# Optimization experiments

Hardware: AMD Instinct MI355X
Metric: run time of the kernel (lower is better)

Reference implementation:

```python
import jax, jax.numpy as jnp
import numpy as np

NUM_HEADS = 16
NEG_FILL = -10000.0  # matches torch masked_fill value in source


def setup_inputs() -> dict:
    key = jax.random.key(0)
    ks = jax.random.split(key, 8)
    B, S, H = 4, 2048, 1024
    sc = 1.0 / np.sqrt(H)
    x = jax.random.normal(ks[0], (B, S, H), dtype=jnp.float32)
    L = jax.random.randint(ks[1], (B,), 1, S + 1, dtype=jnp.int64 if jax.config.jax_enable_x64 else jnp.int32)
    Wq = jax.random.normal(ks[2], (H, H), dtype=jnp.float32) * sc
    Wk = jax.random.normal(ks[3], (H, H), dtype=jnp.float32) * sc
    Wv = jax.random.normal(ks[4], (H, H), dtype=jnp.float32) * sc
    bv = jax.random.normal(ks[5], (H,), dtype=jnp.float32) * 0.01
    Wo = jax.random.normal(ks[6], (H, H), dtype=jnp.float32) * sc
    bo = jax.random.normal(ks[7], (H,), dtype=jnp.float32) * 0.01
    return {"x": x, "L": L, "Wq": Wq, "Wk": Wk, "Wv": Wv, "bv": bv, "Wo": Wo, "bo": bo}


def reference(x, L, Wq, Wk, Wv, bv, Wo, bo):
    # AttentionAggregator.forward with L given; dropout in eval mode (identity).
    B, S, H = x.shape
    nh = NUM_HEADS
    dk = H // nh
    # torch nn.Linear: y = x @ W.T + b
    q = (x @ Wq.T).reshape(B, S, nh, dk).transpose(0, 2, 1, 3)  # (B,h,S,dk)
    k = (x @ Wk.T).reshape(B, S, nh, dk).transpose(0, 2, 1, 3)
    v = (x @ Wv.T + bv).reshape(B, S, nh, dk).transpose(0, 2, 1, 3)
    scores = jnp.einsum("bhqd,bhkd->bhqk", q, k) / jnp.sqrt(jnp.float32(dk))
    valid = jnp.arange(S)[None, :] < L[:, None]  # (B,S) True where real token
    scores = jnp.where(valid[:, None, None, :], scores, NEG_FILL)
    attn = jax.nn.softmax(scores, axis=-1)
    ctx = jnp.einsum("bhqk,bhkd->bhqd", attn, v)
    ctx = ctx.transpose(0, 2, 1, 3).reshape(B, S, H)
    attn_out = ctx @ Wo.T + bo  # (B,S,H)
    # masked mean pool over valid positions
    m = valid.astype(x.dtype)  # (B,S)
    pooled = jnp.einsum("bsh,bs->bh", attn_out, m) / m.sum(axis=1, keepdims=True)
    return pooled
```

## Files before the change

kernel.cpp:

```cpp
#include <hip/hip_runtime.h>
#include <hip/hip_bf16.h>
#include <math.h>

constexpr int Bc = 4, Sc = 2048, Hc = 1024, NHc = 16, DKc = 64;

constexpr size_t XHOFF = 0;
constexpr size_t QOFF  = 4194304;
constexpr size_t KOFF  = 8388608;
constexpr size_t WQOFF = 12582912;
constexpr size_t WKOFF = 13107200;
constexpr size_t LIOFF = 13631488;
constexpr size_t WOFF  = 13762560;
constexpr size_t YOFF  = 13893632;
constexpr size_t CSOFF = 13959168;
constexpr size_t YPOFF = 13963264;
constexpr size_t RPOFF = 13963264;
constexpr size_t CPOFF = 13963264;

typedef __attribute__((ext_vector_type(8))) short bf16x8;
typedef __attribute__((ext_vector_type(4))) float f32x4;

__device__ inline short f2bf(float v) {
    __hip_bfloat16 h = __float2bfloat16(v);
    return *reinterpret_cast<short*>(&h);
}

__device__ inline float ex2(float x) {
#if defined(__has_builtin) && __has_builtin(__builtin_amdgcn_exp2f)
    return __builtin_amdgcn_exp2f(x);
#else
    float r; asm("v_exp_f32 %0, %1" : "=v"(r) : "v"(x)); return r;
#endif
}

__device__ inline void gld_lds16(const void* g, void* l) {
    __builtin_amdgcn_global_load_lds(
        (const __attribute__((address_space(1))) unsigned int*)g,
        (__attribute__((address_space(3))) unsigned int*)l, 16, 0, 0);
}

__global__ __launch_bounds__(256) void cvt_all_kernel(
    const float* __restrict__ x, const float* __restrict__ Wq,
    const float* __restrict__ Wk, float* __restrict__ ws)
{
    const size_t i = ((size_t)blockIdx.x * 256 + threadIdx.x) * 8;
    const float* src; short* dst; float scale; size_t off;
    constexpr float QSC = 0.125f * 1.44269504088896340736f;
    if (i < 8388608)       { src = x;  dst = (short*)(ws + XHOFF); off = i;            scale = 1.0f; }
    else if (i < 9437184)  { src = Wq; dst = (short*)(ws + WQOFF); off = i - 8388608;  scale = QSC;  }
    else                   { src = Wk; dst = (short*)(ws + WKOFF); off = i - 9437184;  scale = 1.0f; }
    float4 a = *(const float4*)(src + off);
    float4 b = *(const float4*)(src + off + 4);
    bf16x8 o;
    o[0] = f2bf(a.x * scale); o[1] = f2bf(a.y * scale);
    o[2] = f2bf(a.z * scale); o[3] = f2bf(a.w * scale);
    o[4] = f2bf(b.x * scale); o[5] = f2bf(b.y * scale);
    o[6] = f2bf(b.z * scale); o[7] = f2bf(b.w * scale);
    *(bf16x8*)(dst + off) = o;
}

__global__ __launch_bounds__(256) void proj_mfma_kernel(
    const int* __restrict__ L, float* __restrict__ ws)
{
    const int z  = blockIdx.z;
    const int m0 = blockIdx.y * 128;
    const int n0 = blockIdx.x * 128;
    const int b  = m0 >> 11;
    const int s0 = m0 & 2047;
    const int Lb = L[b];
    if (s0 >= Lb) return;

    const short* __restrict__ A = (const short*)(ws + XHOFF);
    const short* __restrict__ W = (const short*)(ws + (z == 0 ? WQOFF : WKOFF));
    short* __restrict__ Out = (short*)(ws + (z == 0 ? QOFF : KOFF));

    __shared__ __align__(16) short As[128 * 32];
    __shared__ __align__(16) short Bs[128 * 32];

    const int tid  = threadIdx.x;
    const int lane = tid & 63;
    const int wave = tid >> 6;
    const int l16  = lane & 15, quad = lane >> 4;
    const int wm = (wave & 1) * 64, wn = (wave >> 1) * 64;

    const int c0 = tid, c1 = tid + 256;
    const int r0 = c0 >> 2, g0 = (c0 & 3) * 8;
    const int r1 = c1 >> 2, g1 = (c1 & 3) * 8;
    short* lA0 = As + wave * 512;
    short* lA1 = As + 2048 + wave * 512;
    short* lB0 = Bs + wave * 512;
    short* lB1 = Bs + 2048 + wave * 512;

    const f32x4 z4 = {0.f, 0.f, 0.f, 0.f};
    f32x4 acc[4][4];
    #pragma unroll
    for (int i = 0; i < 4; ++i)
        #pragma unroll
        for (int j = 0; j < 4; ++j) acc[i][j] = z4;

    for (int k0 = 0; k0 < Hc; k0 += 32) {
        __syncthreads();
        gld_lds16(A + (size_t)(m0 + r0) * Hc + k0 + g0, lA0);
        gld_lds16(A + (size_t)(m0 + r1) * Hc + k0 + g1, lA1);
        gld_lds16(W + (size_t)(n0 + r0) * Hc + k0 + g0, lB0);
        gld_lds16(W + (size_t)(n0 + r1) * Hc + k0 + g1, lB1);
        __syncthreads();

        bf16x8 af[4], bfr[4];
        #pragma unroll
        for (int mt = 0; mt < 4; ++mt)
            af[mt] = *(const bf16x8*)(As + (wm + mt * 16 + l16) * 32 + quad * 8);
        #pragma unroll
        for (int nt = 0; nt < 4; ++nt)
            bfr[nt] = *(const bf16x8*)(Bs + (wn + nt * 16 + l16) * 32 + quad * 8);
        #pragma unroll
        for (int mt = 0; mt < 4; ++mt)
            #pragma unroll
            for (int nt = 0; nt < 4; ++nt)
                acc[mt][nt] = __builtin_amdgcn_mfma_f32_16x16x32_bf16(
                    af[mt], bfr[nt], acc[mt][nt], 0, 0, 0);
    }

    #pragma unroll
    for (int mt = 0; mt < 4; ++mt) {
        #pragma unroll
        for (int nt = 0; nt < 4; ++nt) {
            const int n = n0 + wn + nt * 16 + l16;
            const int h = n >> 6, d = n & 63;
            #pragma unroll
            for (int r = 0; r < 4; ++r) {
                const int s = s0 + wm + mt * 16 + quad * 4 + r;
                Out[(((size_t)b * NHc + h) * Sc + s) * DKc + d] =
                    f2bf(acc[mt][nt][r]);
            }
        }
    }
}

__global__ __launch_bounds__(256) void rowsum_part_kernel(
    const int* __restrict__ L, float* __restrict__ ws)
{
    const int bh = blockIdx.x;
    const int b  = bh >> 4;
    const int Lb = L[b];
    const int kc0 = blockIdx.z * 128;
    if (blockIdx.y * 128 >= Lb || kc0 >= Lb) return;

    const int tid  = threadIdx.x;
    const int wave = tid >> 6;
    const int lane = tid & 63;
    const int q0 = blockIdx.y * 128 + wave * 32;
    const int l16 = lane & 15, quad = lane >> 4;

    const short* __restrict__ qarr = (const short*)(ws + QOFF) + (size_t)bh * Sc * DKc;
    const short* __restrict__ karr = (const short*)(ws + KOFF) + (size_t)bh * Sc * DKc;

    __shared__ __align__(16) short Ks[128 * 64];

    const short* qrow0 = qarr + (size_t)(q0 + l16) * DKc;
    const short* qrow1 = qarr + (size_t)(q0 + 16 + l16) * DKc;
    const bf16x8 b0lo = *(const bf16x8*)(qrow0 + quad * 8);
    const bf16x8 b0hi = *(const bf16x8*)(qrow0 + 32 + quad * 8);
    const bf16x8 b1lo = *(const bf16x8*)(qrow1 + quad * 8);
    const bf16x8 b1hi = *(const bf16x8*)(qrow1 + 32 + quad * 8);

    #pragma unroll
    for (int i = 0; i < 4; ++i) {
        const int s = i * 256 + tid;
        const int row = s >> 3, cc = s & 7, c = cc ^ (row & 7);
        gld_lds16(karr + (size_t)(kc0 + row) * DKc + c * 8,
                  Ks + (i * 256 + wave * 64) * 8);
    }
    __syncthreads();

    float lacc0 = 0.f, lacc1 = 0.f;
    if (kc0 + 128 <= Lb) {
        #pragma unroll
        for (int t = 0; t < 8; ++t) {
            const int r = t * 16 + l16;
            const bf16x8 alo = *(const bf16x8*)(Ks + (r * 8 + (quad ^ (r & 7))) * 8);
            const bf16x8 ahi = *(const bf16x8*)(Ks + (r * 8 + ((4 + quad) ^ (r & 7))) * 8);
            f32x4 c0 = {0.f, 0.f, 0.f, 0.f}, c1 = {0.f, 0.f, 0.f, 0.f};
            c0 = __builtin_amdgcn_mfma_f32_16x16x32_bf16(alo, b0lo, c0, 0, 0, 0);
            c0 = __builtin_amdgcn_mfma_f32_16x16x32_bf16(ahi, b0hi, c0, 0, 0, 0);
            c1 = __builtin_amdgcn_mfma_f32_16x16x32_bf16(alo, b1lo, c1, 0, 0, 0);
            c1 = __builtin_amdgcn_mfma_f32_16x16x32_bf16(ahi, b1hi, c1, 0, 0, 0);
            const float e0 = ex2(c0[0]), e1 = ex2(c0[1]), e2 = ex2(c0[2]), e3 = ex2(c0[3]);
            const float f0 = ex2(c1[0]), f1 = ex2(c1[1]), f2 = ex2(c1[2]), f3 = ex2(c1[3]);
            lacc0 += (e0 + e1) + (e2 + e3);
            lacc1 += (f0 + f1) + (f2 + f3);
        }
    } else {
        #pragma unroll
        for (int t = 0; t < 8; ++t) {
            const int r = t * 16 + l16;
            const bf16x8 alo = *(const bf16x8*)(Ks + (r * 8 + (quad ^ (r & 7))) * 8);
            const bf16x8 ahi = *(const bf16x8*)(Ks + (r * 8 + ((4 + quad) ^ (r & 7))) * 8);
            f32x4 c0 = {0.f, 0.f, 0.f, 0.f}, c1 = {0.f, 0.f, 0.f, 0.f};
            c0 = __builtin_amdgcn_mfma_f32_16x16x32_bf16(alo, b0lo, c0, 0, 0, 0);
            c0 = __builtin_amdgcn_mfma_f32_16x16x32_bf16(ahi, b0hi, c0, 0, 0, 0);
            c1 = __builtin_amdgcn_mfma_f32_16x16x32_bf16(alo, b1lo, c1, 0, 0, 0);
            c1 = __builtin_amdgcn_mfma_f32_16x16x32_bf16(ahi, b1hi, c1, 0, 0, 0);
            #pragma unroll
            for (int rr = 0; rr < 4; ++rr) {
                const bool kv = (kc0 + t * 16 + quad * 4 + rr) < Lb;
                lacc0 += kv ? ex2(c0[rr]) : 0.f;
                lacc1 += kv ? ex2(c1[rr]) : 0.f;
            }
        }
    }
    lacc0 += __shfl_xor(lacc0, 16, 64); lacc0 += __shfl_xor(lacc0, 32, 64);
    lacc1 += __shfl_xor(lacc1, 16, 64); lacc1 += __shfl_xor(lacc1, 32, 64);
    float* __restrict__ rp = ws + RPOFF + ((size_t)blockIdx.z * 64 + bh) * Sc;
    if (quad == 0) rp[q0 + l16]      = lacc0;
    if (quad == 1) rp[q0 + 16 + l16] = lacc1;
}

__global__ __launch_bounds__(256) void rowsum_reduce_kernel(
    const int* __restrict__ L, float* __restrict__ ws)
{
    const int bh = blockIdx.y;
    const int q  = blockIdx.x * 256 + threadIdx.x;
    const int nc = (L[bh >> 4] + 127) >> 7;
    float acc = 0.f;
    for (int c = 0; c < nc; ++c)
        acc += ws[RPOFF + ((size_t)c * 64 + bh) * Sc + q];
    ws[LIOFF + (size_t)bh * Sc + q] = 1.0f / acc;
}

__global__ __launch_bounds__(256) void colsum_part_kernel(
    const int* __restrict__ L, float* __restrict__ ws)
{
    const int bh = blockIdx.x;
    const int b  = bh >> 4;
    const int Lb = L[b];
    const int qc0 = blockIdx.z * 128;
    if (blockIdx.y * 128 >= Lb || qc0 >= Lb) return;

    const int tid  = threadIdx.x;
    const int wave = tid >> 6;
    const int lane = tid & 63;
    const int k0 = blockIdx.y * 128 + wave * 32;
    const int l16 = lane & 15, quad = lane >> 4;

    const short* __restrict__ qarr = (const short*)(ws + QOFF) + (size_t)bh * Sc * DKc;
    const short* __restrict__ karr = (const short*)(ws + KOFF) + (size_t)bh * Sc * DKc;
    const float* __restrict__ liarr = ws + LIOFF + (size_t)bh * Sc;

    __shared__ __align__(16) short Qs[128 * 64];
    __shared__ __align__(16) float Lis[128];

    const short* krow0 = karr + (size_t)(k0 + l16) * DKc;
    const short* krow1 = karr + (size_t)(k0 + 16 + l16) * DKc;
    const bf16x8 a0lo = *(const bf16x8*)(krow0 + quad * 8);
    const bf16x8 a0hi = *(const bf16x8*)(krow0 + 32 + quad * 8);
    const bf16x8 a1lo = *(const bf16x8*)(krow1 + quad * 8);
    const bf16x8 a1hi = *(const bf16x8*)(krow1 + 32 + quad * 8);

    #pragma unroll
    for (int i = 0; i < 4; ++i) {
        const int s = i * 256 + tid;
        const int row = s >> 3, cc = s & 7, c = cc ^ (row & 7);
        gld_lds16(qarr + (size_t)(qc0 + row) * DKc + c * 8,
                  Qs + (i * 256 + wave * 64) * 8);
    }
    if (tid < 32)
        gld_lds16(liarr + qc0 + tid * 4, Lis);
    __syncthreads();

    float w0[4] = {0.f, 0.f, 0.f, 0.f};
    float w1[4] = {0.f, 0.f, 0.f, 0.f};

    if (qc0 + 128 <= Lb) {
        #pragma unroll
        for (int t = 0; t < 8; ++t) {
            const int r = t * 16 + l16;
            const bf16x8 blo = *(const bf16x8*)(Qs + (r * 8 + (quad ^ (r & 7))) * 8);
            const bf16x8 bhi = *(const bf16x8*)(Qs + (r * 8 + ((4 + quad) ^ (r & 7))) * 8);
            const float lv = Lis[r];
            f32x4 c0 = {0.f, 0.f, 0.f, 0.f}, c1 = {0.f, 0.f, 0.f, 0.f};
            c0 = __builtin_amdgcn_mfma_f32_16x16x32_bf16(a0lo, blo, c0, 0, 0, 0);
            c0 = __builtin_amdgcn_mfma_f32_16x16x32_bf16(a0hi, bhi, c0, 0, 0, 0);
            c1 = __builtin_amdgcn_mfma_f32_16x16x32_bf16(a1lo, blo, c1, 0, 0, 0);
            c1 = __builtin_amdgcn_mfma_f32_16x16x32_bf16(a1hi, bhi, c1, 0, 0, 0);
            #pragma unroll
            for (int rr = 0; rr < 4; ++rr) {
                w0[rr] += ex2(c0[rr]) * lv;
                w1[rr] += ex2(c1[rr]) * lv;
            }
        }
    } else {
        #pragma unroll
        for (int t = 0; t < 8; ++t) {
            const int r = t * 16 + l16;
            const bf16x8 blo = *(const bf16x8*)(Qs + (r * 8 + (quad ^ (r & 7))) * 8);
            const bf16x8 bhi = *(const bf16x8*)(Qs + (r * 8 + ((4 + quad) ^ (r & 7))) * 8);
            const float lv = (qc0 + r < Lb) ? Lis[r] : 0.f;
            f32x4 c0 = {0.f, 0.f, 0.f, 0.f}, c1 = {0.f, 0.f, 0.f, 0.f};
            c0 = __builtin_amdgcn_mfma_f32_16x16x32_bf16(a0lo, blo, c0, 0, 0, 0);
            c0 = __builtin_amdgcn_mfma_f32_16x16x32_bf16(a0hi, bhi, c0, 0, 0, 0);
            c1 = __builtin_amdgcn_mfma_f32_16x16x32_bf16(a1lo, blo, c1, 0, 0, 0);
            c1 = __builtin_amdgcn_mfma_f32_16x16x32_bf16(a1hi, bhi, c1, 0, 0, 0);
            #pragma unroll
            for (int rr = 0; rr < 4; ++rr) {
                w0[rr] += ex2(c0[rr]) * lv;
                w1[rr] += ex2(c1[rr]) * lv;
            }
        }
    }
    #pragma unroll
    for (int off = 1; off <= 8; off <<= 1) {
        #pragma unroll
        for (int rr = 0; rr < 4; ++rr) {
            w0[rr] += __shfl_xor(w0[rr], off, 64);
            w1[rr] += __shfl_xor(w1[rr], off, 64);
        }
    }
    if (l16 == 0) {
        float* __restrict__ cp = ws + CPOFF + ((size_t)blockIdx.z * 64 + bh) * Sc;
        #pragma unroll
        for (int rr = 0; rr < 4; ++rr) {
            cp[k0 + quad * 4 + rr]      = w0[rr];
            cp[k0 + 16 + quad * 4 + rr] = w1[rr];
        }
    }
}

__global__ __launch_bounds__(256) void colsum_reduce_kernel(
    const int* __restrict__ L, float* __restrict__ ws)
{
    const int bh = blockIdx.y;
    const int k  = blockIdx.x * 256 + threadIdx.x;
    const int nc = (L[bh >> 4] + 127) >> 7;
    float acc = 0.f;
    for (int c = 0; c < nc; ++c)
        acc += ws[CPOFF + ((size_t)c * 64 + bh) * Sc + k];
    ws[WOFF + (size_t)bh * Sc + k] = acc;
}

__global__ __launch_bounds__(256) void yw_part_kernel(
    const float* __restrict__ x, const int* __restrict__ L,
    float* __restrict__ ws)
{
    const int b  = blockIdx.y;
    const int j0 = blockIdx.x * 64;
    const int s0 = blockIdx.z * 128;
    const int Lb = L[b];
    if (s0 >= Lb) return;
    const int js = threadIdx.x & 63;
    const int sl = threadIdx.x >> 6;
    const float* __restrict__ warr = ws + WOFF + (size_t)b * NHc * Sc;
    const float* __restrict__ xb = x + (size_t)b * Sc * Hc;

    __shared__ float wt[128][20];
    __shared__ float red[4][16][64];

    #pragma unroll
    for (int i = 0; i < 8; ++i) {
        const int s = (threadIdx.x & 15) + 16 * i;
        const int h = threadIdx.x >> 4;
        float v = 0.f;
        if (s0 + s < Lb) v = warr[(size_t)h * Sc + s0 + s];
        wt[s][h] = v;
    }
    __syncthreads();

    float acc[16];
    #pragma unroll
    for (int h = 0; h < 16; ++h) acc[h] = 0.f;

    #pragma unroll 4
    for (int s = sl; s < 128; s += 4) {
        const float xv = xb[(size_t)(s0 + s) * Hc + j0 + js];
        const f32x4 wa = *(const f32x4*)&wt[s][0];
        const f32x4 wb = *(const f32x4*)&wt[s][4];
        const f32x4 wc = *(const f32x4*)&wt[s][8];
        const f32x4 wd = *(const f32x4*)&wt[s][12];
        #pragma unroll
        for (int h = 0; h < 4; ++h) acc[h]      += wa[h] * xv;
        #pragma unroll
        for (int h = 0; h < 4; ++h) acc[4 + h]  += wb[h] * xv;
        #pragma unroll
        for (int h = 0; h < 4; ++h) acc[8 + h]  += wc[h] * xv;
        #pragma unroll
        for (int h = 0; h < 4; ++h) acc[12 + h] += wd[h] * xv;
    }
    #pragma unroll
    for (int h = 0; h < 16; ++h) red[sl][h][js] = acc[h];
    __syncthreads();
    if (sl == 0) {
        float* __restrict__ yp = ws + YPOFF +
            ((size_t)blockIdx.z * Bc * NHc + (size_t)b * NHc) * Hc;
        #pragma unroll
        for (int h = 0; h < 16; ++h)
            yp[(size_t)h * Hc + j0 + js] =
                red[0][h][js] + red[1][h][js] + red[2][h][js] + red[3][h][js];
    }
}

__global__ __launch_bounds__(256) void yw_reduce_kernel(
    const int* __restrict__ L, float* __restrict__ ws)
{
    const int b = blockIdx.y;
    const int i = blockIdx.x * 256 + threadIdx.x;
    const int nc = (L[b] + 127) >> 7;
    const float* __restrict__ p = ws + YPOFF + (size_t)b * NHc * Hc + i;
    float acc = 0.f;
    for (int c = 0; c < nc; ++c)
        acc += p[(size_t)c * Bc * NHc * Hc];
    ws[YOFF + (size_t)b * NHc * Hc + i] = acc;
}

__global__ __launch_bounds__(256) void csum_kernel(
    const float* __restrict__ Wv, const float* __restrict__ bv,
    const int* __restrict__ L, float* __restrict__ ws)
{
    const int b = blockIdx.y;
    const int h = blockIdx.x;
    const int n0 = h * 64;
    const int lane = threadIdx.x & 63;
    const int wave = threadIdx.x >> 6;
    const float Lb = (float)L[b];

    __shared__ float ys[1024];
    const float* __restrict__ y = ws + YOFF + ((size_t)b * NHc + h) * Hc;
    for (int i = threadIdx.x; i < 1024; i += 256) ys[i] = y[i];
    __syncthreads();

    f32x4 yv[4];
    #pragma unroll
    for (int p = 0; p < 4; ++p) yv[p] = *(const f32x4*)&ys[p * 256 + lane * 4];

    #pragma unroll
    for (int r = 0; r < 16; ++r) {
        const int n = n0 + wave * 16 + r;
        const float* wrow = Wv + (size_t)n * Hc;
        float a = 0.f;
        #pragma unroll
        for (int p = 0; p < 4; ++p) {
            const f32x4 wv = *(const f32x4*)(wrow + p * 256 + lane * 4);
            a += wv[0]*yv[p][0] + wv[1]*yv[p][1] + wv[2]*yv[p][2] + wv[3]*yv[p][3];
        }
        #pragma unroll
        for (int off = 32; off > 0; off >>= 1) a += __shfl_xor(a, off, 64);
        if (lane == 0)
            ws[CSOFF + (size_t)b * Hc + n] = a + bv[n] * Lb;
    }
}

__global__ __launch_bounds__(256) void out_kernel(
    const float* __restrict__ Wo, const float* __restrict__ bo,
    const int* __restrict__ L, const float* __restrict__ ws,
    float* __restrict__ out)
{
    const int b = blockIdx.y;
    const int o0 = blockIdx.x * 64;
    const int lane = threadIdx.x & 63;
    const int wave = threadIdx.x >> 6;
    const float linv = 1.0f / (float)L[b];

    __shared__ float cs[1024];
    const float* __restrict__ c = ws + CSOFF + (size_t)b * Hc;
    for (int i = threadIdx.x; i < 1024; i += 256) cs[i] = c[i];
    __syncthreads();

    f32x4 cv[4];
    #pragma unroll
    for (int p = 0; p < 4; ++p) cv[p] = *(const f32x4*)&cs[p * 256 + lane * 4];

    #pragma unroll
    for (int r = 0; r < 16; ++r) {
        const int o = o0 + wave * 16 + r;
        const float* wrow = Wo + (size_t)o * Hc;
        float a = 0.f;
        #pragma unroll
        for (int p = 0; p < 4; ++p) {
            const f32x4 wv = *(const f32x4*)(wrow + p * 256 + lane * 4);
            a += wv[0]*cv[p][0] + wv[1]*cv[p][1] + wv[2]*cv[p][2] + wv[3]*cv[p][3];
        }
        #pragma unroll
        for (int off = 32; off > 0; off >>= 1) a += __shfl_xor(a, off, 64);
        if (lane == 0)
            out[(size_t)b * Hc + o] = a * linv + bo[o];
    }
}

extern "C" void kernel_launch(void* const* d_in, const int* in_sizes, int n_in,
                              void* d_out, int out_size, void* d_ws, size_t ws_size,
                              hipStream_t stream)
{
    (void)in_sizes; (void)n_in; (void)out_size; (void)ws_size;
    const float* x  = (const float*)d_in[0];
    const int*   L  = (const int*)d_in[1];
    const float* Wq = (const float*)d_in[2];
    const float* Wk = (const float*)d_in[3];
    const float* Wv = (const float*)d_in[4];
    const float* bv = (const float*)d_in[5];
    const float* Wo = (const float*)d_in[6];
    const float* bo = (const float*)d_in[7];
    float* out = (float*)d_out;
    float* ws  = (float*)d_ws;

    cvt_all_kernel<<<5120, 256, 0, stream>>>(x, Wq, Wk, ws);

    dim3 gp(Hc / 128, (Bc * Sc) / 128, 2);
    proj_mfma_kernel<<<gp, 256, 0, stream>>>(L, ws);

    dim3 gr(Bc * NHc, Sc / 128, 16);
    rowsum_part_kernel<<<gr, 256, 0, stream>>>(L, ws);
    dim3 grr(Sc / 256, Bc * NHc);
    rowsum_reduce_kernel<<<grr, 256, 0, stream>>>(L, ws);

    dim3 gcp(Bc * NHc, Sc / 128, 16);
    colsum_part_kernel<<<gcp, 256, 0, stream>>>(L, ws);
    colsum_reduce_kernel<<<grr, 256, 0, stream>>>(L, ws);

    dim3 gy(Hc / 64, Bc, Sc / 128);
    yw_part_kernel<<<gy, 256, 0, stream>>>(x, L, ws);

    dim3 gyr((NHc * Hc) / 256, Bc);
    yw_reduce_kernel<<<gyr, 256, 0, stream>>>(L, ws);

    dim3 gc(NHc, Bc);
    csum_kernel<<<gc, 256, 0, stream>>>(Wv, bv, L, ws);

    dim3 go(Hc / 64, Bc);
    out_kernel<<<go, 256, 0, stream>>>(Wo, bo, L, ws, out);
}
```

Baseline: 240.9 us.

## Loop over four double-buffered K/Q tiles per block in rowsum/colsum kernels

Each rowsum and colsum partial block now covers 512 keys or queries instead of 128. It loops over four 128-row tiles, prefetching the next tile into a second LDS buffer with explicit vmcnt waits and barriers. The split-K grid shrinks from 16 to 4 chunks, so the reduce kernels read fewer partials and the per-block Q or K fragment loads are amortised over more work. The cost is double the LDS per block and fewer, longer blocks, which may reduce parallelism when L is short.

```diff
diff --git a/kernel.cpp b/kernel.cpp
--- a/kernel.cpp
+++ b/kernel.cpp
@@ -143,7 +143,7 @@
     const int bh = blockIdx.x;
     const int b  = bh >> 4;
     const int Lb = L[b];
-    const int kc0 = blockIdx.z * 128;
+    const int kc0 = blockIdx.z * 512;
     if (blockIdx.y * 128 >= Lb || kc0 >= Lb) return;
 
     const int tid  = threadIdx.x;
@@ -155,7 +155,7 @@
     const short* __restrict__ qarr = (const short*)(ws + QOFF) + (size_t)bh * Sc * DKc;
     const short* __restrict__ karr = (const short*)(ws + KOFF) + (size_t)bh * Sc * DKc;
 
-    __shared__ __align__(16) short Ks[128 * 64];
+    __shared__ __align__(16) short Ks[2][128 * 64];
 
     const short* qrow0 = qarr + (size_t)(q0 + l16) * DKc;
     const short* qrow1 = qarr + (size_t)(q0 + 16 + l16) * DKc;
@@ -164,51 +164,72 @@
     const bf16x8 b1lo = *(const bf16x8*)(qrow1 + quad * 8);
     const bf16x8 b1hi = *(const bf16x8*)(qrow1 + 32 + quad * 8);
 
-    #pragma unroll
-    for (int i = 0; i < 4; ++i) {
-        const int s = i * 256 + tid;
-        const int row = s >> 3, cc = s & 7, c = cc ^ (row & 7);
-        gld_lds16(karr + (size_t)(kc0 + row) * DKc + c * 8,
-                  Ks + (i * 256 + wave * 64) * 8);
-    }
-    __syncthreads();
-
+    const int kend  = (kc0 + 512 < Lb) ? kc0 + 512 : Lb;
+    const int ntile = (kend - kc0 + 127) >> 7;
+
+    auto stage = [&](int bufi, int kt) {
+        short* dst = &Ks[bufi][0];
+        #pragma unroll
+        for (int i = 0; i < 4; ++i) {
+            const int s = i * 256 + tid;
+            const int row = s >> 3, c = (s & 7) ^ (row & 7);
+            gld_lds16(karr + (size_t)(kt + row) * DKc + c * 8,
+                      dst + (i * 256 + wave * 64) * 8);
+        }
+    };
+
+    stage(0, kc0);
     float lacc0 = 0.f, lacc1 = 0.f;
-    if (kc0 + 128 <= Lb) {
-        #pragma unroll
-        for (int t = 0; t < 8; ++t) {
-            const int r = t * 16 + l16;
-            const bf16x8 alo = *(const bf16x8*)(Ks + (r * 8 + (quad ^ (r & 7))) * 8);
-            const bf16x8 ahi = *(const bf16x8*)(Ks + (r * 8 + ((4 + quad) ^ (r & 7))) * 8);
-            f32x4 c0 = {0.f, 0.f, 0.f, 0.f}, c1 = {0.f, 0.f, 0.f, 0.f};
-            c0 = __builtin_amdgcn_mfma_f32_16x16x32_bf16(alo, b0lo, c0, 0, 0, 0);
-            c0 = __builtin_amdgcn_mfma_f32_16x16x32_bf16(ahi, b0hi, c0, 0, 0, 0);
-            c1 = __builtin_amdgcn_mfma_f32_16x16x32_bf16(alo, b1lo, c1, 0, 0, 0);
-            c1 = __builtin_amdgcn_mfma_f32_16x16x32_bf16(ahi, b1hi, c1, 0, 0, 0);
-            const float e0 = ex2(c0[0]), e1 = ex2(c0[1]), e2 = ex2(c0[2]), e3 = ex2(c0[3]);
-            const float f0 = ex2(c1[0]), f1 = ex2(c1[1]), f2 = ex2(c1[2]), f3 = ex2(c1[3]);
-            lacc0 += (e0 + e1) + (e2 + e3);
-            lacc1 += (f0 + f1) + (f2 + f3);
-        }
-    } else {
-        #pragma unroll
-        for (int t = 0; t < 8; ++t) {
-            const int r = t * 16 + l16;
-            const bf16x8 alo = *(const bf16x8*)(Ks + (r * 8 + (quad ^ (r & 7))) * 8);
-            const bf16x8 ahi = *(const bf16x8*)(Ks + (r * 8 + ((4 + quad) ^ (r & 7))) * 8);
-            f32x4 c0 = {0.f, 0.f, 0.f, 0.f}, c1 = {0.f, 0.f, 0.f, 0.f};
-            c0 = __builtin_amdgcn_mfma_f32_16x16x32_bf16(alo, b0lo, c0, 0, 0, 0);
-            c0 = __builtin_amdgcn_mfma_f32_16x16x32_bf16(ahi, b0hi, c0, 0, 0, 0);
-            c1 = __builtin_amdgcn_mfma_f32_16x16x32_bf16(alo, b1lo, c1, 0, 0, 0);
-            c1 = __builtin_amdgcn_mfma_f32_16x16x32_bf16(ahi, b1hi, c1, 0, 0, 0);
+
+    for (int t = 0; t < ntile; ++t) {
+        const int kt = kc0 + t * 128;
+        if (t + 1 < ntile) {
+            stage((t + 1) & 1, kt + 128);
+            asm volatile("s_waitcnt vmcnt(4)" ::: "memory");
+        } else {
+            asm volatile("s_waitcnt vmcnt(0)" ::: "memory");
+        }
+        __builtin_amdgcn_s_barrier();
+
+        const short* Kt = &Ks[t & 1][0];
+        if (kt + 128 <= Lb) {
             #pragma unroll
-            for (int rr = 0; rr < 4; ++rr) {
-                const bool kv = (kc0 + t * 16 + quad * 4 + rr) < Lb;
-                lacc0 += kv ? ex2(c0[rr]) : 0.f;
-                lacc1 += kv ? ex2(c1[rr]) : 0.f;
+            for (int tt = 0; tt < 8; ++tt) {
+                const int r = tt * 16 + l16;
+                const bf16x8 alo = *(const bf16x8*)(Kt + (r * 8 + (quad ^ (r & 7))) * 8);
+                const bf16x8 ahi = *(const bf16x8*)(Kt + (r * 8 + ((4 + quad) ^ (r & 7))) * 8);
+                f32x4 c0 = {0.f, 0.f, 0.f, 0.f}, c1 = {0.f, 0.f, 0.f, 0.f};
+                c0 = __builtin_amdgcn_mfma_f32_16x16x32_bf16(alo, b0lo, c0, 0, 0, 0);
+                c0 = __builtin_amdgcn_mfma_f32_16x16x32_bf16(ahi, b0hi, c0, 0, 0, 0);
+                c1 = __builtin_amdgcn_mfma_f32_16x16x32_bf16(alo, b1lo, c1, 0, 0, 0);
+                c1 = __builtin_amdgcn_mfma_f32_16x16x32_bf16(ahi, b1hi, c1, 0, 0, 0);
+                const float e0 = ex2(c0[0]), e1 = ex2(c0[1]), e2 = ex2(c0[2]), e3 = ex2(c0[3]);
+                const float f0 = ex2(c1[0]), f1 = ex2(c1[1]), f2 = ex2(c1[2]), f3 = ex2(c1[3]);
+                lacc0 += (e0 + e1) + (e2 + e3);
+                lacc1 += (f0 + f1) + (f2 + f3);
             }
-        }
-    }
+        } else {
+            #pragma unroll
+            for (int tt = 0; tt < 8; ++tt) {
+                const int r = tt * 16 + l16;
+                const bf16x8 alo = *(const bf16x8*)(Kt + (r * 8 + (quad ^ (r & 7))) * 8);
+                const bf16x8 ahi = *(const bf16x8*)(Kt + (r * 8 + ((4 + quad) ^ (r & 7))) * 8);
+                f32x4 c0 = {0.f, 0.f, 0.f, 0.f}, c1 = {0.f, 0.f, 0.f, 0.f};
+                c0 = __builtin_amdgcn_mfma_f32_16x16x32_bf16(alo, b0lo, c0, 0, 0, 0);
+                c0 = __builtin_amdgcn_mfma_f32_16x16x32_bf16(ahi, b0hi, c0, 0, 0, 0);
+                c1 = __builtin_amdgcn_mfma_f32_16x16x32_bf16(alo, b1lo, c1, 0, 0, 0);
+                c1 = __builtin_amdgcn_mfma_f32_16x16x32_bf16(ahi, b1hi, c1, 0, 0, 0);
+                #pragma unroll
+                for (int rr = 0; rr < 4; ++rr) {
+                    const bool kv = (kt + tt * 16 + quad * 4 + rr) < Lb;
+                    lacc0 += kv ? ex2(c0[rr]) : 0.f;
+                    lacc1 += kv ? ex2(c1[rr]) : 0.f;
+                }
+            }
+        }
+        __builtin_amdgcn_s_barrier();
+    }
+
     lacc0 += __shfl_xor(lacc0, 16, 64); lacc0 += __shfl_xor(lacc0, 32, 64);
     lacc1 += __shfl_xor(lacc1, 16, 64); lacc1 += __shfl_xor(lacc1, 32, 64);
     float* __restrict__ rp = ws + RPOFF + ((size_t)blockIdx.z * 64 + bh) * Sc;
@@ -221,7 +242,7 @@
 {
     const int bh = blockIdx.y;
     const int q  = blockIdx.x * 256 + threadIdx.x;
-    const int nc = (L[bh >> 4] + 127) >> 7;
+    const int nc = (L[bh >> 4] + 511) >> 9;
     float acc = 0.f;
     for (int c = 0; c < nc; ++c)
         acc += ws[RPOFF + ((size_t)c * 64 + bh) * Sc + q];
@@ -234,7 +255,7 @@
     const int bh = blockIdx.x;
     const int b  = bh >> 4;
     const int Lb = L[b];
-    const int qc0 = blockIdx.z * 128;
+    const int qc0 = blockIdx.z * 512;
     if (blockIdx.y * 128 >= Lb || qc0 >= Lb) return;
 
     const int tid  = threadIdx.x;
@@ -247,8 +268,8 @@
     const short* __restrict__ karr = (const short*)(ws + KOFF) + (size_t)bh * Sc * DKc;
     const float* __restrict__ liarr = ws + LIOFF + (size_t)bh * Sc;
 
-    __shared__ __align__(16) short Qs[128 * 64];
-    __shared__ __align__(16) float Lis[128];
+    __shared__ __align__(16) short Qs[2][128 * 64];
+    __shared__ __align__(16) float Lis[2][128];
 
     const short* krow0 = karr + (size_t)(k0 + l16) * DKc;
     const short* krow1 = karr + (size_t)(k0 + 16 + l16) * DKc;
@@ -257,57 +278,79 @@
     const bf16x8 a1lo = *(const bf16x8*)(krow1 + quad * 8);
     const bf16x8 a1hi = *(const bf16x8*)(krow1 + 32 + quad * 8);
 
-    #pragma unroll
-    for (int i = 0; i < 4; ++i) {
-        const int s = i * 256 + tid;
-        const int row = s >> 3, cc = s & 7, c = cc ^ (row & 7);
-        gld_lds16(qarr + (size_t)(qc0 + row) * DKc + c * 8,
-                  Qs + (i * 256 + wave * 64) * 8);
-    }
-    if (tid < 32)
-        gld_lds16(liarr + qc0 + tid * 4, Lis);
-    __syncthreads();
-
+    const int qend  = (qc0 + 512 < Lb) ? qc0 + 512 : Lb;
+    const int ntile = (qend - qc0 + 127) >> 7;
+
+    auto stage = [&](int bufi, int qt) {
+        short* dst = &Qs[bufi][0];
+        #pragma unroll
+        for (int i = 0; i < 4; ++i) {
+            const int s = i * 256 + tid;
+            const int row = s >> 3, c = (s & 7) ^ (row & 7);
+            gld_lds16(qarr + (size_t)(qt + row) * DKc + c * 8,
+                      dst + (i * 256 + wave * 64) * 8);
+        }
+        if (tid < 32)
+            gld_lds16(liarr + qt + tid * 4, &Lis[bufi][0]);
+    };
+
+    stage(0, qc0);
     float w0[4] = {0.f, 0.f, 0.f, 0.f};
     float w1[4] = {0.f, 0.f, 0.f, 0.f};
 
-    if (qc0 + 128 <= Lb) {
-        #pragma unroll
-        for (int t = 0; t < 8; ++t) {
-            const int r = t * 16 + l16;
-            const bf16x8 blo = *(const bf16x8*)(Qs + (r * 8 + (quad ^ (r & 7))) * 8);
-            const bf16x8 bhi = *(const bf16x8*)(Qs + (r * 8 + ((4 + quad) ^ (r & 7))) * 8);
-            const float lv = Lis[r];
-            f32x4 c0 = {0.f, 0.f, 0.f, 0.f}, c1 = {0.f, 0.f, 0.f, 0.f};
-            c0 = __builtin_amdgcn_mfma_f32_16x16x32_bf16(a0lo, blo, c0, 0, 0, 0);
-            c0 = __builtin_amdgcn_mfma_f32_16x16x32_bf16(a0hi, bhi, c0, 0, 0, 0);
-            c1 = __builtin_amdgcn_mfma_f32_16x16x32_bf16(a1lo, blo, c1, 0, 0, 0);
-            c1 = __builtin_amdgcn_mfma_f32_16x16x32_bf16(a1hi, bhi, c1, 0, 0, 0);
+    for (int t = 0; t < ntile; ++t) {
+        const int qt = qc0 + t * 128;
+        if (t + 1 < ntile) {
+            stage((t + 1) & 1, qt + 128);
+            if (wave == 0) asm volatile("s_waitcnt vmcnt(5)" ::: "memory");
+            else           asm volatile("s_waitcnt vmcnt(4)" ::: "memory");
+        } else {
+            asm volatile("s_waitcnt vmcnt(0)" ::: "memory");
+        }
+        __builtin_amdgcn_s_barrier();
+
+        const short* Qt = &Qs[t & 1][0];
+        const float* Lt = &Lis[t & 1][0];
+        if (qt + 128 <= Lb) {
             #pragma unroll
-            for (int rr = 0; rr < 4; ++rr) {
-                w0[rr] += ex2(c0[rr]) * lv;
-                w1[rr] += ex2(c1[rr]) * lv;
+            for (int tt = 0; tt < 8; ++tt) {
+                const int r = tt * 16 + l16;
+                const bf16x8 blo = *(const bf16x8*)(Qt + (r * 8 + (quad ^ (r & 7))) * 8);
+                const bf16x8 bhi = *(const bf16x8*)(Qt + (r * 8 + ((4 + quad) ^ (r & 7))) * 8);
+                const float lv = Lt[r];
+                f32x4 c0 = {0.f, 0.f, 0.f, 0.f}, c1 = {0.f, 0.f, 0.f, 0.f};
+                c0 = __builtin_amdgcn_mfma_f32_16x16x32_bf16(a0lo, blo, c0, 0, 0, 0);
+                c0 = __builtin_amdgcn_mfma_f32_16x16x32_bf16(a0hi, bhi, c0, 0, 0, 0);
+                c1 = __builtin_amdgcn_mfma_f32_16x16x32_bf16(a1lo, blo, c1, 0, 0, 0);
+                c1 = __builtin_amdgcn_mfma_f32_16x16x32_bf16(a1hi, bhi, c1, 0, 0, 0);
+                #pragma unroll
+                for (int rr = 0; rr < 4; ++rr) {
+                    w0[rr] += ex2(c0[rr]) * lv;
+                    w1[rr] += ex2(c1[rr]) * lv;
+                }
             }
-        }
-    } else {
-        #pragma unroll
-        for (int t = 0; t < 8; ++t) {
-            const int r = t * 16 + l16;
-            const bf16x8 blo = *(const bf16x8*)(Qs + (r * 8 + (quad ^ (r & 7))) * 8);
-            const bf16x8 bhi = *(const bf16x8*)(Qs + (r * 8 + ((4 + quad) ^ (r & 7))) * 8);
-            const float lv = (qc0 + r < Lb) ? Lis[r] : 0.f;
-            f32x4 c0 = {0.f, 0.f, 0.f, 0.f}, c1 = {0.f, 0.f, 0.f, 0.f};
-            c0 = __builtin_amdgcn_mfma_f32_16x16x32_bf16(a0lo, blo, c0, 0, 0, 0);
-            c0 = __builtin_amdgcn_mfma_f32_16x16x32_bf16(a0hi, bhi, c0, 0, 0, 0);
-            c1 = __builtin_amdgcn_mfma_f32_16x16x32_bf16(a1lo, blo, c1, 0, 0, 0);
-            c1 = __builtin_amdgcn_mfma_f32_16x16x32_bf16(a1hi, bhi, c1, 0, 0, 0);
+        } else {
             #pragma unroll
-            for (int rr = 0; rr < 4; ++rr) {
-                w0[rr] += ex2(c0[rr]) * lv;
-                w1[rr] += ex2(c1[rr]) * lv;
+            for (int tt = 0; tt < 8; ++tt) {
+                const int r = tt * 16 + l16;
+                const bf16x8 blo = *(const bf16x8*)(Qt + (r * 8 + (quad ^ (r & 7))) * 8);
+                const bf16x8 bhi = *(const bf16x8*)(Qt + (r * 8 + ((4 + quad) ^ (r & 7))) * 8);
+                const float lv = (qt + r < Lb) ? Lt[r] : 0.f;
+                f32x4 c0 = {0.f, 0.f, 0.f, 0.f}, c1 = {0.f, 0.f, 0.f, 0.f};
+                c0 = __builtin_amdgcn_mfma_f32_16x16x32_bf16(a0lo, blo, c0, 0, 0, 0);
+                c0 = __builtin_amdgcn_mfma_f32_16x16x32_bf16(a0hi, bhi, c0, 0, 0, 0);
+                c1 = __builtin_amdgcn_mfma_f32_16x16x32_bf16(a1lo, blo, c1, 0, 0, 0);
+                c1 = __builtin_amdgcn_mfma_f32_16x16x32_bf16(a1hi, bhi, c1, 0, 0, 0);
+                #pragma unroll
+                for (int rr = 0; rr < 4; ++rr) {
+                    w0[rr] += ex2(c0[rr]) * lv;
+                    w1[rr] += ex2(c1[rr]) * lv;
+                }
             }
         }
-    }
+        __builtin_amdgcn_s_barrier();
+    }
+
     #pragma unroll
     for (int off = 1; off <= 8; off <<= 1) {
         #pragma unroll
@@ -331,7 +374,7 @@
 {
     const int bh = blockIdx.y;
     const int k  = blockIdx.x * 256 + threadIdx.x;
-    const int nc = (L[bh >> 4] + 127) >> 7;
+    const int nc = (L[bh >> 4] + 511) >> 9;
     float acc = 0.f;
     for (int c = 0; c < nc; ++c)
         acc += ws[CPOFF + ((size_t)c * 64 + bh) * Sc + k];
@@ -506,12 +549,12 @@
     dim3 gp(Hc / 128, (Bc * Sc) / 128, 2);
     proj_mfma_kernel<<<gp, 256, 0, stream>>>(L, ws);
 
-    dim3 gr(Bc * NHc, Sc / 128, 16);
+    dim3 gr(Bc * NHc, Sc / 128, 4);
     rowsum_part_kernel<<<gr, 256, 0, stream>>>(L, ws);
     dim3 grr(Sc / 256, Bc * NHc);
     rowsum_reduce_kernel<<<grr, 256, 0, stream>>>(L, ws);
 
-    dim3 gcp(Bc * NHc, Sc / 128, 16);
+    dim3 gcp(Bc * NHc, Sc / 128, 4);
     colsum_part_kernel<<<gcp, 256, 0, stream>>>(L, ws);
     colsum_reduce_kernel<<<grr, 256, 0, stream>>>(L, ws);
 
```

Measured after the change: 230.4 us. 4.3% less time.

## Make rowsum/colsum kernels persistent per-wave with direct global loads

Applied to the files above, without the earlier changes.

Rewrites the rowsum and colsum partial kernels as persistent grids of 1024 blocks. Each wave independently loops over (head, 64-row group, 128-column chunk) work items and skips items past the valid length L. The LDS staging and block barriers are removed; each wave keeps 4 groups of Q (or K) fragments in registers and streams the other operand directly from global/L2. This aims to remove the many early-exit blocks, barrier overhead and idle waves under ragged lengths, and to balance load across CUs. The cost is more register pressure and redundant global reads of K/Q rows, since there is no longer any shared-memory reuse across waves.

```diff
diff --git a/kernel.cpp b/kernel.cpp
--- a/kernel.cpp
+++ b/kernel.cpp
@@ -137,83 +137,80 @@
     }
 }
 
-__global__ __launch_bounds__(256) void rowsum_part_kernel(
-    const int* __restrict__ L, float* __restrict__ ws)
-{
-    const int bh = blockIdx.x;
-    const int b  = bh >> 4;
-    const int Lb = L[b];
-    const int kc0 = blockIdx.z * 128;
-    if (blockIdx.y * 128 >= Lb || kc0 >= Lb) return;
-
-    const int tid  = threadIdx.x;
-    const int wave = tid >> 6;
-    const int lane = tid & 63;
-    const int q0 = blockIdx.y * 128 + wave * 32;
+__global__ __launch_bounds__(256, 4) void rowsum_part_kernel(
+    const int* __restrict__ L, float* __restrict__ ws)
+{
+    const int wid  = blockIdx.x * 4 + (threadIdx.x >> 6);
+    const int lane = threadIdx.x & 63;
     const int l16 = lane & 15, quad = lane >> 4;
-
-    const short* __restrict__ qarr = (const short*)(ws + QOFF) + (size_t)bh * Sc * DKc;
-    const short* __restrict__ karr = (const short*)(ws + KOFF) + (size_t)bh * Sc * DKc;
-
-    __shared__ __align__(16) short Ks[128 * 64];
-
-    const short* qrow0 = qarr + (size_t)(q0 + l16) * DKc;
-    const short* qrow1 = qarr + (size_t)(q0 + 16 + l16) * DKc;
-    const bf16x8 b0lo = *(const bf16x8*)(qrow0 + quad * 8);
-    const bf16x8 b0hi = *(const bf16x8*)(qrow0 + 32 + quad * 8);
-    const bf16x8 b1lo = *(const bf16x8*)(qrow1 + quad * 8);
-    const bf16x8 b1hi = *(const bf16x8*)(qrow1 + 32 + quad * 8);
-
-    #pragma unroll
-    for (int i = 0; i < 4; ++i) {
-        const int s = i * 256 + tid;
-        const int row = s >> 3, cc = s & 7, c = cc ^ (row & 7);
-        gld_lds16(karr + (size_t)(kc0 + row) * DKc + c * 8,
-                  Ks + (i * 256 + wave * 64) * 8);
-    }
-    __syncthreads();
-
-    float lacc0 = 0.f, lacc1 = 0.f;
-    if (kc0 + 128 <= Lb) {
-        #pragma unroll
-        for (int t = 0; t < 8; ++t) {
-            const int r = t * 16 + l16;
-            const bf16x8 alo = *(const bf16x8*)(Ks + (r * 8 + (quad ^ (r & 7))) * 8);
-            const bf16x8 ahi = *(const bf16x8*)(Ks + (r * 8 + ((4 + quad) ^ (r & 7))) * 8);
-            f32x4 c0 = {0.f, 0.f, 0.f, 0.f}, c1 = {0.f, 0.f, 0.f, 0.f};
-            c0 = __builtin_amdgcn_mfma_f32_16x16x32_bf16(alo, b0lo, c0, 0, 0, 0);
-            c0 = __builtin_amdgcn_mfma_f32_16x16x32_bf16(ahi, b0hi, c0, 0, 0, 0);
-            c1 = __builtin_amdgcn_mfma_f32_16x16x32_bf16(alo, b1lo, c1, 0, 0, 0);
-            c1 = __builtin_amdgcn_mfma_f32_16x16x32_bf16(ahi, b1hi, c1, 0, 0, 0);
-            const float e0 = ex2(c0[0]), e1 = ex2(c0[1]), e2 = ex2(c0[2]), e3 = ex2(c0[3]);
-            const float f0 = ex2(c1[0]), f1 = ex2(c1[1]), f2 = ex2(c1[2]), f3 = ex2(c1[3]);
-            lacc0 += (e0 + e1) + (e2 + e3);
-            lacc1 += (f0 + f1) + (f2 + f3);
-        }
-    } else {
-        #pragma unroll
-        for (int t = 0; t < 8; ++t) {
-            const int r = t * 16 + l16;
-            const bf16x8 alo = *(const bf16x8*)(Ks + (r * 8 + (quad ^ (r & 7))) * 8);
-            const bf16x8 ahi = *(const bf16x8*)(Ks + (r * 8 + ((4 + quad) ^ (r & 7))) * 8);
-            f32x4 c0 = {0.f, 0.f, 0.f, 0.f}, c1 = {0.f, 0.f, 0.f, 0.f};
-            c0 = __builtin_amdgcn_mfma_f32_16x16x32_bf16(alo, b0lo, c0, 0, 0, 0);
-            c0 = __builtin_amdgcn_mfma_f32_16x16x32_bf16(ahi, b0hi, c0, 0, 0, 0);
-            c1 = __builtin_amdgcn_mfma_f32_16x16x32_bf16(alo, b1lo, c1, 0, 0, 0);
-            c1 = __builtin_amdgcn_mfma_f32_16x16x32_bf16(ahi, b1hi, c1, 0, 0, 0);
-            #pragma unroll
-            for (int rr = 0; rr < 4; ++rr) {
-                const bool kv = (kc0 + t * 16 + quad * 4 + rr) < Lb;
-                lacc0 += kv ? ex2(c0[rr]) : 0.f;
-                lacc1 += kv ? ex2(c1[rr]) : 0.f;
+    const int L0 = L[0], L1 = L[1], L2 = L[2], L3 = L[3];
+    const short* __restrict__ qbase = (const short*)(ws + QOFF);
+    const short* __restrict__ kbase = (const short*)(ws + KOFF);
+
+    for (int it = wid; it < 32768; it += 4096) {
+        const int bh = it & 63;
+        const int qg = (it >> 6) & 31;
+        const int zc = it >> 11;
+        const int b  = bh >> 4;
+        const int Lb = (b == 0) ? L0 : (b == 1) ? L1 : (b == 2) ? L2 : L3;
+        const int q0 = qg * 64, kt = zc * 128;
+        if (q0 >= Lb || kt >= Lb) continue;
+
+        const short* __restrict__ qarr = qbase + (size_t)bh * Sc * DKc;
+        const short* __restrict__ karr = kbase + (size_t)bh * Sc * DKc;
+
+        bf16x8 bq[4][2];
+        #pragma unroll
+        for (int g = 0; g < 4; ++g) {
+            const short* qr = qarr + (size_t)(q0 + g * 16 + l16) * DKc;
+            bq[g][0] = *(const bf16x8*)(qr + quad * 8);
+            bq[g][1] = *(const bf16x8*)(qr + 32 + quad * 8);
+        }
+        float lac[4] = {0.f, 0.f, 0.f, 0.f};
+
+        if (kt + 128 <= Lb) {
+            #pragma unroll
+            for (int tt = 0; tt < 8; ++tt) {
+                const short* kr = karr + (size_t)(kt + tt * 16 + l16) * DKc;
+                const bf16x8 alo = *(const bf16x8*)(kr + quad * 8);
+                const bf16x8 ahi = *(const bf16x8*)(kr + 32 + quad * 8);
+                #pragma unroll
+                for (int g = 0; g < 4; ++g) {
+                    f32x4 c = {0.f, 0.f, 0.f, 0.f};
+                    c = __builtin_amdgcn_mfma_f32_16x16x32_bf16(alo, bq[g][0], c, 0, 0, 0);
+                    c = __builtin_amdgcn_mfma_f32_16x16x32_bf16(ahi, bq[g][1], c, 0, 0, 0);
+                    lac[g] += (ex2(c[0]) + ex2(c[1])) + (ex2(c[2]) + ex2(c[3]));
+                }
             }
-        }
-    }
-    lacc0 += __shfl_xor(lacc0, 16, 64); lacc0 += __shfl_xor(lacc0, 32, 64);
-    lacc1 += __shfl_xor(lacc1, 16, 64); lacc1 += __shfl_xor(lacc1, 32, 64);
-    float* __restrict__ rp = ws + RPOFF + ((size_t)blockIdx.z * 64 + bh) * Sc;
-    if (quad == 0) rp[q0 + l16]      = lacc0;
-    if (quad == 1) rp[q0 + 16 + l16] = lacc1;
+        } else {
+            #pragma unroll
+            for (int tt = 0; tt < 8; ++tt) {
+                const short* kr = karr + (size_t)(kt + tt * 16 + l16) * DKc;
+                const bf16x8 alo = *(const bf16x8*)(kr + quad * 8);
+                const bf16x8 ahi = *(const bf16x8*)(kr + 32 + quad * 8);
+                #pragma unroll
+                for (int g = 0; g < 4; ++g) {
+                    f32x4 c = {0.f, 0.f, 0.f, 0.f};
+                    c = __builtin_amdgcn_mfma_f32_16x16x32_bf16(alo, bq[g][0], c, 0, 0, 0);
+                    c = __builtin_amdgcn_mfma_f32_16x16x32_bf16(ahi, bq[g][1], c, 0, 0, 0);
+                    #pragma unroll
+                    for (int rr = 0; rr < 4; ++rr) {
+                        const bool kv = (kt + tt * 16 + quad * 4 + rr) < Lb;
+                        lac[g] += kv ? ex2(c[rr]) : 0.f;
+                    }
+                }
+            }
+        }
+        #pragma unroll
+        for (int g = 0; g < 4; ++g) {
+            lac[g] += __shfl_xor(lac[g], 16, 64);
+            lac[g] += __shfl_xor(lac[g], 32, 64);
+        }
+        float* __restrict__ rp = ws + RPOFF + ((size_t)zc * 64 + bh) * Sc;
+        #pragma unroll
+        for (int g = 0; g < 4; ++g)
+            if (quad == g) rp[q0 + g * 16 + l16] = lac[g];
+    }
 }
 
 __global__ __launch_bounds__(256) void rowsum_reduce_kernel(
@@ -228,100 +225,91 @@
     ws[LIOFF + (size_t)bh * Sc + q] = 1.0f / acc;
 }
 
-__global__ __launch_bounds__(256) void colsum_part_kernel(
-    const int* __restrict__ L, float* __restrict__ ws)
-{
-    const int bh = blockIdx.x;
-    const int b  = bh >> 4;
-    const int Lb = L[b];
-    const int qc0 = blockIdx.z * 128;
-    if (blockIdx.y * 128 >= Lb || qc0 >= Lb) return;
-
-    const int tid  = threadIdx.x;
-    const int wave = tid >> 6;
-    const int lane = tid & 63;
-    const int k0 = blockIdx.y * 128 + wave * 32;
+__global__ __launch_bounds__(256, 4) void colsum_part_kernel(
+    const int* __restrict__ L, float* __restrict__ ws)
+{
+    const int wid  = blockIdx.x * 4 + (threadIdx.x >> 6);
+    const int lane = threadIdx.x & 63;
     const int l16 = lane & 15, quad = lane >> 4;
-
-    const short* __restrict__ qarr = (const short*)(ws + QOFF) + (size_t)bh * Sc * DKc;
-    const short* __restrict__ karr = (const short*)(ws + KOFF) + (size_t)bh * Sc * DKc;
-    const float* __restrict__ liarr = ws + LIOFF + (size_t)bh * Sc;
-
-    __shared__ __align__(16) short Qs[128 * 64];
-    __shared__ __align__(16) float Lis[128];
-
-    const short* krow0 = karr + (size_t)(k0 + l16) * DKc;
-    const short* krow1 = karr + (size_t)(k0 + 16 + l16) * DKc;
-    const bf16x8 a0lo = *(const bf16x8*)(krow0 + quad * 8);
-    const bf16x8 a0hi = *(const bf16x8*)(krow0 + 32 + quad * 8);
-    const bf16x8 a1lo = *(const bf16x8*)(krow1 + quad * 8);
-    const bf16x8 a1hi = *(const bf16x8*)(krow1 + 32 + quad * 8);
-
-    #pragma unroll
-    for (int i = 0; i < 4; ++i) {
-        const int s = i * 256 + tid;
-        const int row = s >> 3, cc = s & 7, c = cc ^ (row & 7);
-        gld_lds16(qarr + (size_t)(qc0 + row) * DKc + c * 8,
-                  Qs + (i * 256 + wave * 64) * 8);
-    }
-    if (tid < 32)
-        gld_lds16(liarr + qc0 + tid * 4, Lis);
-    __syncthreads();
-
-    float w0[4] = {0.f, 0.f, 0.f, 0.f};
-    float w1[4] = {0.f, 0.f, 0.f, 0.f};
-
-    if (qc0 + 128 <= Lb) {
-        #pragma unroll
-        for (int t = 0; t < 8; ++t) {
-            const int r = t * 16 + l16;
-            const bf16x8 blo = *(const bf16x8*)(Qs + (r * 8 + (quad ^ (r & 7))) * 8);
-            const bf16x8 bhi = *(const bf16x8*)(Qs + (r * 8 + ((4 + quad) ^ (r & 7))) * 8);
-            const float lv = Lis[r];
-            f32x4 c0 = {0.f, 0.f, 0.f, 0.f}, c1 = {0.f, 0.f, 0.f, 0.f};
-            c0 = __builtin_amdgcn_mfma_f32_16x16x32_bf16(a0lo, blo, c0, 0, 0, 0);
-            c0 = __builtin_amdgcn_mfma_f32_16x16x32_bf16(a0hi, bhi, c0, 0, 0, 0);
-            c1 = __builtin_amdgcn_mfma_f32_16x16x32_bf16(a1lo, blo, c1, 0, 0, 0);
-            c1 = __builtin_amdgcn_mfma_f32_16x16x32_bf16(a1hi, bhi, c1, 0, 0, 0);
-            #pragma unroll
-            for (int rr = 0; rr < 4; ++rr) {
-                w0[rr] += ex2(c0[rr]) * lv;
-                w1[rr] += ex2(c1[rr]) * lv;
+    const int L0 = L[0], L1 = L[1], L2 = L[2], L3 = L[3];
+    const short* __restrict__ qbase = (const short*)(ws + QOFF);
+    const short* __restrict__ kbase = (const short*)(ws + KOFF);
+
+    for (int it = wid; it < 32768; it += 4096) {
+        const int bh = it & 63;
+        const int kg = (it >> 6) & 31;
+        const int zq = it >> 11;
+        const int b  = bh >> 4;
+        const int Lb = (b == 0) ? L0 : (b == 1) ? L1 : (b == 2) ? L2 : L3;
+        const int k0 = kg * 64, qt = zq * 128;
+        if (k0 >= Lb || qt >= Lb) continue;
+
+        const short* __restrict__ qarr = qbase + (size_t)bh * Sc * DKc;
+        const short* __restrict__ karr = kbase + (size_t)bh * Sc * DKc;
+        const float* __restrict__ li = ws + LIOFF + (size_t)bh * Sc;
+
+        bf16x8 ak[4][2];
+        #pragma unroll
+        for (int g = 0; g < 4; ++g) {
+            const short* kr = karr + (size_t)(k0 + g * 16 + l16) * DKc;
+            ak[g][0] = *(const bf16x8*)(kr + quad * 8);
+            ak[g][1] = *(const bf16x8*)(kr + 32 + quad * 8);
+        }
+        f32x4 w[4];
+        #pragma unroll
+        for (int g = 0; g < 4; ++g) w[g] = (f32x4){0.f, 0.f, 0.f, 0.f};
+
+        if (qt + 128 <= Lb) {
+            #pragma unroll
+            for (int tt = 0; tt < 8; ++tt) {
+                const int qrow = qt + tt * 16 + l16;
+                const short* qr = qarr + (size_t)qrow * DKc;
+                const bf16x8 blo = *(const bf16x8*)(qr + quad * 8);
+                const bf16x8 bhi = *(const bf16x8*)(qr + 32 + quad * 8);
+                const float lv = li[qrow];
+                #pragma unroll
+                for (int g = 0; g < 4; ++g) {
+                    f32x4 c = {0.f, 0.f, 0.f, 0.f};
+                    c = __builtin_amdgcn_mfma_f32_16x16x32_bf16(ak[g][0], blo, c, 0, 0, 0);
+                    c = __builtin_amdgcn_mfma_f32_16x16x32_bf16(ak[g][1], bhi, c, 0, 0, 0);
+                    #pragma unroll
+                    for (int rr = 0; rr < 4; ++rr)
+                        w[g][rr] += ex2(c[rr]) * lv;
+                }
             }
-        }
-    } else {
-        #pragma unroll
-        for (int t = 0; t < 8; ++t) {
-            const int r = t * 16 + l16;
-            const bf16x8 blo = *(const bf16x8*)(Qs + (r * 8 + (quad ^ (r & 7))) * 8);
-            const bf16x8 bhi = *(const bf16x8*)(Qs + (r * 8 + ((4 + quad) ^ (r & 7))) * 8);
-            const float lv = (qc0 + r < Lb) ? Lis[r] : 0.f;
-            f32x4 c0 = {0.f, 0.f, 0.f, 0.f}, c1 = {0.f, 0.f, 0.f, 0.f};
-            c0 = __builtin_amdgcn_mfma_f32_16x16x32_bf16(a0lo, blo, c0, 0, 0, 0);
-            c0 = __builtin_amdgcn_mfma_f32_16x16x32_bf16(a0hi, bhi, c0, 0, 0, 0);
-            c1 = __builtin_amdgcn_mfma_f32_16x16x32_bf16(a1lo, blo, c1, 0, 0, 0);
-            c1 = __builtin_amdgcn_mfma_f32_16x16x32_bf16(a1hi, bhi, c1, 0, 0, 0);
-            #pragma unroll
-            for (int rr = 0; rr < 4; ++rr) {
-                w0[rr] += ex2(c0[rr]) * lv;
-                w1[rr] += ex2(c1[rr]) * lv;
+        } else {
+            #pragma unroll
+            for (int tt = 0; tt < 8; ++tt) {
+                const int qrow = qt + tt * 16 + l16;
+                const short* qr = qarr + (size_t)qrow * DKc;
+                const bf16x8 blo = *(const bf16x8*)(qr + quad * 8);
+                const bf16x8 bhi = *(const bf16x8*)(qr + 32 + quad * 8);
+                const float lv = (qrow < Lb) ? li[qrow] : 0.f;
+                #pragma unroll
+                for (int g = 0; g < 4; ++g) {
+                    f32x4 c = {0.f, 0.f, 0.f, 0.f};
+                    c = __builtin_amdgcn_mfma_f32_16x16x32_bf16(ak[g][0], blo, c, 0, 0, 0);
+                    c = __builtin_amdgcn_mfma_f32_16x16x32_bf16(ak[g][1], bhi, c, 0, 0, 0);
+                    #pragma unroll
+                    for (int rr = 0; rr < 4; ++rr)
+                        w[g][rr] += ex2(c[rr]) * lv;
+                }
             }
         }
-    }
-    #pragma unroll
-    for (int off = 1; off <= 8; off <<= 1) {
-        #pragma unroll
-        for (int rr = 0; rr < 4; ++rr) {
-            w0[rr] += __shfl_xor(w0[rr], off, 64);
-            w1[rr] += __shfl_xor(w1[rr], off, 64);
-        }
-    }
-    if (l16 == 0) {
-        float* __restrict__ cp = ws + CPOFF + ((size_t)blockIdx.z * 64 + bh) * Sc;
-        #pragma unroll
-        for (int rr = 0; rr < 4; ++rr) {
-            cp[k0 + quad * 4 + rr]      = w0[rr];
-            cp[k0 + 16 + quad * 4 + rr] = w1[rr];
+        #pragma unroll
+        for (int off = 1; off <= 8; off <<= 1)
+            #pragma unroll
+            for (int g = 0; g < 4; ++g)
+                #pragma unroll
+                for (int rr = 0; rr < 4; ++rr)
+                    w[g][rr] += __shfl_xor(w[g][rr], off, 64);
+        float* __restrict__ cp = ws + CPOFF + ((size_t)zq * 64 + bh) * Sc;
+        if (l16 == 0) {
+            #pragma unroll
+            for (int g = 0; g < 4; ++g)
+                #pragma unroll
+                for (int rr = 0; rr < 4; ++rr)
+                    cp[k0 + g * 16 + quad * 4 + rr] = w[g][rr];
         }
     }
 }
@@ -506,13 +494,11 @@
     dim3 gp(Hc / 128, (Bc * Sc) / 128, 2);
     proj_mfma_kernel<<<gp, 256, 0, stream>>>(L, ws);
 
-    dim3 gr(Bc * NHc, Sc / 128, 16);
-    rowsum_part_kernel<<<gr, 256, 0, stream>>>(L, ws);
+    rowsum_part_kernel<<<1024, 256, 0, stream>>>(L, ws);
     dim3 grr(Sc / 256, Bc * NHc);
     rowsum_reduce_kernel<<<grr, 256, 0, stream>>>(L, ws);
 
-    dim3 gcp(Bc * NHc, Sc / 128, 16);
-    colsum_part_kernel<<<gcp, 256, 0, stream>>>(L, ws);
+    colsum_part_kernel<<<1024, 256, 0, stream>>>(L, ws);
     colsum_reduce_kernel<<<grr, 256, 0, stream>>>(L, ws);
 
     dim3 gy(Hc / 64, Bc, Sc / 128);
```

Result: slower. 427.1 us (+77.3%).
